# Kernel tuning notes

Hardware: AMD Instinct MI355X
Metric: run time of the kernel (lower is better)

The kernel has to match this reference:

```python
import jax, jax.numpy as jnp
import numpy as np

B, C1, C2, K, H, W = 2, 256, 256, 3, 64, 64
PAD = 1
EPS = 1e-5
K2 = K * K
OUT_OFF = 3 * K2  # deform_groups=1: 2*k2 offset channels + k2 mask channels


def setup_inputs() -> dict:
    key = jax.random.key(0)
    ks = jax.random.split(key, 8)
    x = jax.random.normal(ks[0], (B, C1, H, W), jnp.float32)
    # small scale so predicted offsets stay within a few pixels (realistic trained regime)
    w_off = jax.random.normal(ks[1], (OUT_OFF, C1, 3, 3), jnp.float32) * 0.01
    b_off = jax.random.normal(ks[2], (OUT_OFF,), jnp.float32) * 0.01
    w_dcn = jax.random.normal(ks[3], (C2, C1, K, K), jnp.float32) / np.sqrt(C1 * K2).astype(np.float32)
    gamma = 1.0 + 0.1 * jax.random.normal(ks[4], (C2,), jnp.float32)
    beta = 0.1 * jax.random.normal(ks[5], (C2,), jnp.float32)
    run_mean = 0.1 * jax.random.normal(ks[6], (C2,), jnp.float32)
    run_var = jax.random.uniform(ks[7], (C2,), jnp.float32, minval=0.5, maxval=1.5)
    return {"x": x, "w_off": w_off, "b_off": b_off, "w_dcn": w_dcn,
            "gamma": gamma, "beta": beta, "run_mean": run_mean, "run_var": run_var}


def _dcnv2_bn_silu(x, w_off, b_off, w_dcn, gamma, beta, run_mean, run_var):
    # offset/mask predictor: plain 3x3 conv, stride 1, pad 1
    om = jax.lax.conv_general_dilated(x, w_off, (1, 1), [(PAD, PAD), (PAD, PAD)])
    om = om + b_off[None, :, None, None]  # [B, 27, H, W]
    # mmcv channel layout: (dy, dx) interleaved per kernel tap, then mask
    offset = om[:, :2 * K2].reshape(B, K2, 2, H, W)
    mask = jax.nn.sigmoid(om[:, 2 * K2:3 * K2])  # [B, K2, H, W]
    dy, dx = offset[:, :, 0], offset[:, :, 1]     # [B, K2, H, W]

    ki = jnp.arange(K)
    tap_y = jnp.repeat(ki, K)  # [K2]
    tap_x = jnp.tile(ki, K)    # [K2]
    base_y = jnp.arange(H)[None, None, :, None] - PAD + tap_y[None, :, None, None]
    base_x = jnp.arange(W)[None, None, None, :] - PAD + tap_x[None, :, None, None]
    py = base_y.astype(x.dtype) + dy  # [B, K2, H, W] sampling rows
    px = base_x.astype(x.dtype) + dx  # [B, K2, H, W] sampling cols

    y0f = jnp.floor(py)
    x0f = jnp.floor(px)
    ly = (py - y0f)[:, None]  # [B, 1, K2, H, W]
    lx = (px - x0f)[:, None]
    y0 = y0f.astype(jnp.int32)
    x0 = x0f.astype(jnp.int32)

    x_flat = x.reshape(B, C1, H * W)

    def gather(yi, xi):
        valid = ((yi >= 0) & (yi < H) & (xi >= 0) & (xi < W)).astype(x.dtype)
        idx = jnp.clip(yi, 0, H - 1) * W + jnp.clip(xi, 0, W - 1)  # [B, K2, H, W]
        v = jnp.take_along_axis(x_flat, idx.reshape(B, 1, -1), axis=2)
        return v.reshape(B, C1, K2, H, W) * valid[:, None]

    v00 = gather(y0, x0)
    v01 = gather(y0, x0 + 1)
    v10 = gather(y0 + 1, x0)
    v11 = gather(y0 + 1, x0 + 1)
    vals = (v00 * (1 - ly) * (1 - lx) + v01 * (1 - ly) * lx
            + v10 * ly * (1 - lx) + v11 * ly * lx)
    vals = vals * mask[:, None]  # modulated

    out = jnp.einsum('bckhw,ock->bohw', vals, w_dcn.reshape(C2, C1, K2))

    # BatchNorm (inference, running stats) + SiLU
    inv = gamma / jnp.sqrt(run_var + EPS)
    y = out * inv[None, :, None, None] + (beta - run_mean * inv)[None, :, None, None]
    return y * jax.nn.sigmoid(y)


def reference(x, w_off, b_off, w_dcn, gamma, beta, run_mean, run_var):
    return _dcnv2_bn_silu(x, w_off, b_off, w_dcn, gamma, beta, run_mean, run_var)
```

## Files before the change

### kernel.cpp

```cpp
#include <hip/hip_runtime.h>
#include <hip/hip_bf16.h>
#include <math.h>

typedef __bf16 bf16x8 __attribute__((ext_vector_type(8)));
typedef float  f32x4  __attribute__((ext_vector_type(4)));

#define BB 2
#define C1 256
#define C2 256
#define HH 64
#define WW 64
#define HW 4096
#define OCH 27
#define EPSV 1e-5f

#define WBF_OFF  0u
#define WOFF_OFF 1179648u
#define XT_OFF   1327104u

__global__ __launch_bounds__(256) void prep_kernel(
    const float* __restrict__ x, const float* __restrict__ w_dcn,
    const float* __restrict__ w_off, __bf16* __restrict__ xT,
    __bf16* __restrict__ wbfS, __bf16* __restrict__ woffS)
{
    __shared__ __bf16 tile[64][72];
    const int bi = blockIdx.x, tid = threadIdx.x;

    if (bi < 512) {
        const int b = bi >> 8;
        const int ht = (bi & 255) >> 2;
        const int ct = bi & 3;
        const int hw_l = tid & 63, cg = tid >> 6;
        const float* src = x + ((size_t)(b * 256 + ct * 64 + cg * 16) << 12)
                             + ht * 64 + hw_l;
        #pragma unroll
        for (int i = 0; i < 16; i++)
            tile[hw_l][cg * 16 + i] = (__bf16)src[(size_t)i << 12];
        __syncthreads();
        const int hw_o = tid >> 2, cq = tid & 3;
        __bf16* dst = xT + ((size_t)(b * HW + ht * 64 + hw_o) << 8)
                         + ct * 64 + cq * 16;
        *(bf16x8*)dst       = *(const bf16x8*)&tile[hw_o][cq * 16];
        *(bf16x8*)(dst + 8) = *(const bf16x8*)&tile[hw_o][cq * 16 + 8];
    } else if (bi < 800) {
        int t = (bi - 512) * 256 + tid;
        int l = t & 63;
        int nb = (t >> 6) & 15;
        int ks = (t >> 10) & 1;
        int kb = t >> 11;
        int o = nb * 16 + (l & 15);
        int kq = (l >> 4) & 3;
        bf16x8 v;
        #pragma unroll
        for (int j = 0; j < 8; j++) {
            int K = kb * 64 + ks * 32 + kq * 8 + j;
            v[j] = (__bf16)w_dcn[o * 2304 + (K & 255) * 9 + (K >> 8)];
        }
        *(bf16x8*)(wbfS + (size_t)t * 8) = v;
    } else {
        int t = (bi - 800) * 256 + tid;
        int l = t & 63;
        int nf = (t >> 6) & 1;
        int ks = (t >> 7) & 1;
        int kb = t >> 8;
        int o = nf * 16 + (l & 15);
        int kq = (l >> 4) & 3;
        bf16x8 v;
        #pragma unroll
        for (int j = 0; j < 8; j++) {
            int K = kb * 64 + ks * 32 + kq * 8 + j;
            v[j] = (o < OCH) ? (__bf16)w_off[o * 2304 + (K & 255) * 9 + (K >> 8)]
                             : (__bf16)0.f;
        }
        *(bf16x8*)(woffS + (size_t)t * 8) = v;
    }
}

union SU {
    float sD[4][16][33];
    float sC[2][16][136];
};

__global__ __launch_bounds__(256, 4) void fused_kernel(
    const __bf16* __restrict__ xT, const __bf16* __restrict__ wbfS,
    const __bf16* __restrict__ woffS, const float* __restrict__ b_off,
    const float* __restrict__ gamma, const float* __restrict__ beta,
    const float* __restrict__ rmean, const float* __restrict__ rvar,
    float* __restrict__ out)
{
    __shared__ SU u;
    __shared__ float  sOm[32][16];
    __shared__ int4   sO[9][16];
    __shared__ float4 sW[9][16];

    const int tid = threadIdx.x, wv = tid >> 6, lane = tid & 63;
    const int bi = blockIdx.x;
    const int xcd = bi & 7, rr = bi >> 3;
    const int g = xcd * 64 + (rr >> 1);
    const int nHalf = rr & 1;
    const int pixBase = g * 16;
    const int b = pixBase >> 12;
    const int hwBase = pixBase & 4095;
    const int h = hwBase >> 6, w0 = hwBase & 63;
    const int n15 = lane & 15, q4 = lane >> 4;

    const char* xb = (const char*)xT + ((size_t)b << 12) * 512;

    {
        f32x4 acc2[2];
        #pragma unroll
        for (int j = 0; j < 2; j++) acc2[j] = (f32x4){0.f, 0.f, 0.f, 0.f};

        for (int i = 0; i < 9; i++) {
            const int kb = wv * 9 + i;
            const int k = kb >> 2, cc = kb & 3;
            const int kh = k / 3, kw = k % 3;
            const int hh = h + kh - 1;
            const int ww = w0 + n15 + kw - 1;
            const bool valid = (hh >= 0) && (hh < HH) && (ww >= 0) && (ww < WW);
            const int hc = min(max(hh, 0), HH - 1);
            const int wc = min(max(ww, 0), WW - 1);
            const char* src = xb + (size_t)(hc * WW + wc) * 512
                                 + (cc * 64 + q4 * 8) * 2;
            bf16x8 af[2];
            af[0] = *(const bf16x8*)src;
            af[1] = *(const bf16x8*)(src + 64);
            if (!valid) {
                #pragma unroll
                for (int j = 0; j < 8; j++) {
                    af[0][j] = (__bf16)0.f; af[1][j] = (__bf16)0.f;
                }
            }
            #pragma unroll
            for (int nf = 0; nf < 2; nf++) {
                #pragma unroll
                for (int ks = 0; ks < 2; ks++) {
                    bf16x8 bfr = *(const bf16x8*)(woffS
                        + ((size_t)(((kb * 2 + ks) * 2 + nf) * 64 + lane)) * 8);
                    acc2[nf] = __builtin_amdgcn_mfma_f32_16x16x32_bf16(
                        af[ks], bfr, acc2[nf], 0, 0, 0);
                }
            }
        }
        #pragma unroll
        for (int nf = 0; nf < 2; nf++)
            #pragma unroll
            for (int r = 0; r < 4; r++)
                u.sD[wv][q4 * 4 + r][nf * 16 + n15] = acc2[nf][r];
    }
    __syncthreads();
    for (int t = tid; t < OCH * 16; t += 256) {
        int oc = t >> 4, p = t & 15;
        sOm[oc][p] = b_off[oc] + u.sD[0][p][oc] + u.sD[1][p][oc]
                               + u.sD[2][p][oc] + u.sD[3][p][oc];
    }
    __syncthreads();

    if (tid < 144) {
        int k = tid >> 4, p = tid & 15;
        float dy = sOm[2 * k][p];
        float dx = sOm[2 * k + 1][p];
        float mm = sOm[18 + k][p];
        mm = 1.f / (1.f + __expf(-mm));
        float py = (float)(h - 1 + k / 3) + dy;
        float px = (float)(w0 + p - 1 + k % 3) + dx;
        float y0f = floorf(py), x0f = floorf(px);
        float ly = py - y0f, lx = px - x0f;
        int y0 = (int)y0f, x0 = (int)x0f;
        int yc0 = min(max(y0, 0), HH - 1),     yc1 = min(max(y0 + 1, 0), HH - 1);
        int xc0 = min(max(x0, 0), WW - 1),     xc1 = min(max(x0 + 1, 0), WW - 1);
        float vy0 = (y0 >= 0 && y0 < HH) ? 1.f : 0.f;
        float vy1 = (y0 + 1 >= 0 && y0 + 1 < HH) ? 1.f : 0.f;
        float vx0 = (x0 >= 0 && x0 < WW) ? 1.f : 0.f;
        float vx1 = (x0 + 1 >= 0 && x0 + 1 < WW) ? 1.f : 0.f;
        sO[k][p] = (int4){(yc0 * WW + xc0) * 512, (yc0 * WW + xc1) * 512,
                          (yc1 * WW + xc0) * 512, (yc1 * WW + xc1) * 512};
        sW[k][p] = (float4){(1.f - ly) * (1.f - lx) * vy0 * vx0 * mm,
                            (1.f - ly) * lx         * vy0 * vx1 * mm,
                            ly         * (1.f - lx) * vy1 * vx0 * mm,
                            ly         * lx         * vy1 * vx1 * mm};
    }
    __syncthreads();

    f32x4 acc[8];
    #pragma unroll
    for (int j = 0; j < 8; j++) acc[j] = (f32x4){0.f, 0.f, 0.f, 0.f};

    for (int i = 0; i < 9; i++) {
        const int kb = wv * 9 + i;
        const int k = kb >> 2, cc = kb & 3;
        const int4   O = sO[k][n15];
        const float4 W = sW[k][n15];
        const char* base = xb + (cc * 64 + q4 * 8) * 2;

        bf16x8 af[2];
        #pragma unroll
        for (int ks = 0; ks < 2; ks++) {
            const char* bc = base + ks * 64;
            bf16x8 c00 = *(const bf16x8*)(bc + O.x);
            bf16x8 c01 = *(const bf16x8*)(bc + O.y);
            bf16x8 c10 = *(const bf16x8*)(bc + O.z);
            bf16x8 c11 = *(const bf16x8*)(bc + O.w);
            bf16x8 a;
            #pragma unroll
            for (int j = 0; j < 8; j++) {
                float v = W.x * (float)c00[j] + W.y * (float)c01[j]
                        + W.z * (float)c10[j] + W.w * (float)c11[j];
                a[j] = (__bf16)v;
            }
            af[ks] = a;
        }

        #pragma unroll
        for (int half = 0; half < 2; half++) {
            bf16x8 bfr[4][2];
            #pragma unroll
            for (int nb = 0; nb < 4; nb++)
                #pragma unroll
                for (int ks = 0; ks < 2; ks++)
                    bfr[nb][ks] = *(const bf16x8*)(wbfS
                        + ((size_t)(((kb * 2 + ks) * 16 + nHalf * 8 + half * 4 + nb)
                                    * 64 + lane)) * 8);
            #pragma unroll
            for (int nb = 0; nb < 4; nb++)
                #pragma unroll
                for (int ks = 0; ks < 2; ks++)
                    acc[half * 4 + nb] = __builtin_amdgcn_mfma_f32_16x16x32_bf16(
                        af[ks], bfr[nb][ks], acc[half * 4 + nb], 0, 0, 0);
        }
    }

    if (wv < 2) {
        #pragma unroll
        for (int nb = 0; nb < 8; nb++)
            #pragma unroll
            for (int r = 0; r < 4; r++)
                u.sC[wv][q4 * 4 + r][nb * 16 + n15] = acc[nb][r];
    }
    __syncthreads();
    if (wv >= 2) {
        #pragma unroll
        for (int nb = 0; nb < 8; nb++)
            #pragma unroll
            for (int r = 0; r < 4; r++)
                u.sC[wv - 2][q4 * 4 + r][nb * 16 + n15] += acc[nb][r];
    }
    __syncthreads();

    const int px = tid & 15, og = tid >> 4;
    float* ob = out + ((size_t)b * C2 << 12) + hwBase + px;
    #pragma unroll
    for (int ii = 0; ii < 8; ii++) {
        int col = og * 8 + ii;
        int o = nHalf * 128 + col;
        float s = u.sC[0][px][col] + u.sC[1][px][col];
        float inv = gamma[o] * rsqrtf(rvar[o] + EPSV);
        float sh = beta[o] - rmean[o] * inv;
        float y = s * inv + sh;
        ob[(size_t)o << 12] = y * (1.f / (1.f + __expf(-y)));
    }
}

extern "C" void kernel_launch(void* const* d_in, const int* in_sizes, int n_in,
                              void* d_out, int out_size, void* d_ws, size_t ws_size,
                              hipStream_t stream) {
    const float* x      = (const float*)d_in[0];
    const float* w_off  = (const float*)d_in[1];
    const float* b_off  = (const float*)d_in[2];
    const float* w_dcn  = (const float*)d_in[3];
    const float* gamma  = (const float*)d_in[4];
    const float* beta   = (const float*)d_in[5];
    const float* rmean  = (const float*)d_in[6];
    const float* rvar   = (const float*)d_in[7];
    float* out = (float*)d_out;

    char* ws = (char*)d_ws;
    __bf16* wbfS  = (__bf16*)(ws + WBF_OFF);
    __bf16* woffS = (__bf16*)(ws + WOFF_OFF);
    __bf16* xT    = (__bf16*)(ws + XT_OFF);

    prep_kernel<<<836, 256, 0, stream>>>(x, w_dcn, w_off, xT, wbfS, woffS);
    fused_kernel<<<1024, 256, 0, stream>>>(xT, wbfS, woffS, b_off,
                                           gamma, beta, rmean, rvar, out);
}
```

Before: 141.5 us.

## Compute all output channels per block and stage w_dcn repack through LDS

The fused kernel now has each block compute all 256 output channels for its 16 pixels instead of half. This removes the duplicated offset conv, bilinear sampling and gather work that the two channel-half blocks used to repeat, at the cost of twice the accumulator registers and lower occupancy (the occupancy hint in launch bounds is dropped). Separately, the weight repack in the prep kernel now reads w_dcn with coalesced float4 loads into shared memory and scatters from there, replacing strided scalar global reads.

```diff
diff --git a/kernel.cpp b/kernel.cpp
--- a/kernel.cpp
+++ b/kernel.cpp
@@ -24,6 +24,7 @@
     __bf16* __restrict__ wbfS, __bf16* __restrict__ woffS)
 {
     __shared__ __bf16 tile[64][72];
+    __shared__ __bf16 lw[16][584];
     const int bi = blockIdx.x, tid = threadIdx.x;
 
     if (bi < 512) {
@@ -42,23 +43,37 @@
                          + ct * 64 + cq * 16;
         *(bf16x8*)dst       = *(const bf16x8*)&tile[hw_o][cq * 16];
         *(bf16x8*)(dst + 8) = *(const bf16x8*)&tile[hw_o][cq * 16 + 8];
-    } else if (bi < 800) {
-        int t = (bi - 512) * 256 + tid;
-        int l = t & 63;
-        int nb = (t >> 6) & 15;
-        int ks = (t >> 10) & 1;
-        int kb = t >> 11;
-        int o = nb * 16 + (l & 15);
-        int kq = (l >> 4) & 3;
-        bf16x8 v;
-        #pragma unroll
-        for (int j = 0; j < 8; j++) {
-            int K = kb * 64 + ks * 32 + kq * 8 + j;
-            v[j] = (__bf16)w_dcn[o * 2304 + (K & 255) * 9 + (K >> 8)];
-        }
-        *(bf16x8*)(wbfS + (size_t)t * 8) = v;
+    } else if (bi < 576) {
+        const int b2 = bi - 512;
+        const int nb = b2 >> 2, qtr = b2 & 3;
+        #pragma unroll
+        for (int ii = 0; ii < 9; ii++) {
+            int m = tid + 256 * ii;
+            int base = m * 4;
+            int o_l = base / 576;
+            int f = base - o_l * 576;
+            float4 v = *(const float4*)(w_dcn
+                + (size_t)(nb * 16 + o_l) * 2304 + qtr * 576 + f);
+            lw[o_l][f]     = (__bf16)v.x;
+            lw[o_l][f + 1] = (__bf16)v.y;
+            lw[o_l][f + 2] = (__bf16)v.z;
+            lw[o_l][f + 3] = (__bf16)v.w;
+        }
+        __syncthreads();
+        #pragma unroll
+        for (int ii = 0; ii < 36; ii++) {
+            int e = ii * 256 + tid;
+            int seg = e >> 9, s = e & 511;
+            int lane = s >> 3, j = s & 7;
+            int tap = seg >> 1, ks = seg & 1;
+            int kb = tap * 4 + qtr;
+            int o_l = lane & 15, kq = (lane >> 4) & 3;
+            int c_local = ks * 32 + kq * 8 + j;
+            wbfS[((size_t)(((kb * 2 + ks) * 16 + nb) * 64 + lane)) * 8 + j]
+                = lw[o_l][c_local * 9 + tap];
+        }
     } else {
-        int t = (bi - 800) * 256 + tid;
+        int t = (bi - 576) * 256 + tid;
         int l = t & 63;
         int nf = (t >> 6) & 1;
         int ks = (t >> 7) & 1;
@@ -78,10 +93,10 @@
 
 union SU {
     float sD[4][16][33];
-    float sC[2][16][136];
+    float sC[2][16][260];
 };
 
-__global__ __launch_bounds__(256, 4) void fused_kernel(
+__global__ __launch_bounds__(256) void fused_kernel(
     const __bf16* __restrict__ xT, const __bf16* __restrict__ wbfS,
     const __bf16* __restrict__ woffS, const float* __restrict__ b_off,
     const float* __restrict__ gamma, const float* __restrict__ beta,
@@ -94,10 +109,7 @@
     __shared__ float4 sW[9][16];
 
     const int tid = threadIdx.x, wv = tid >> 6, lane = tid & 63;
-    const int bi = blockIdx.x;
-    const int xcd = bi & 7, rr = bi >> 3;
-    const int g = xcd * 64 + (rr >> 1);
-    const int nHalf = rr & 1;
+    const int g = (blockIdx.x & 7) * 64 + (blockIdx.x >> 3);
     const int pixBase = g * 16;
     const int b = pixBase >> 12;
     const int hwBase = pixBase & 4095;
@@ -182,9 +194,9 @@
     }
     __syncthreads();
 
-    f32x4 acc[8];
+    f32x4 acc[16];
     #pragma unroll
-    for (int j = 0; j < 8; j++) acc[j] = (f32x4){0.f, 0.f, 0.f, 0.f};
+    for (int j = 0; j < 16; j++) acc[j] = (f32x4){0.f, 0.f, 0.f, 0.f};
 
     for (int i = 0; i < 9; i++) {
         const int kb = wv * 9 + i;
@@ -213,26 +225,25 @@
 
         #pragma unroll
         for (int half = 0; half < 2; half++) {
-            bf16x8 bfr[4][2];
-            #pragma unroll
-            for (int nb = 0; nb < 4; nb++)
+            bf16x8 bfr[8][2];
+            #pragma unroll
+            for (int nb = 0; nb < 8; nb++)
                 #pragma unroll
                 for (int ks = 0; ks < 2; ks++)
                     bfr[nb][ks] = *(const bf16x8*)(wbfS
-                        + ((size_t)(((kb * 2 + ks) * 16 + nHalf * 8 + half * 4 + nb)
-                                    * 64 + lane)) * 8);
-            #pragma unroll
-            for (int nb = 0; nb < 4; nb++)
+                        + ((size_t)(((kb * 2 + ks) * 16 + half * 8 + nb) * 64 + lane)) * 8);
+            #pragma unroll
+            for (int nb = 0; nb < 8; nb++)
                 #pragma unroll
                 for (int ks = 0; ks < 2; ks++)
-                    acc[half * 4 + nb] = __builtin_amdgcn_mfma_f32_16x16x32_bf16(
-                        af[ks], bfr[nb][ks], acc[half * 4 + nb], 0, 0, 0);
+                    acc[half * 8 + nb] = __builtin_amdgcn_mfma_f32_16x16x32_bf16(
+                        af[ks], bfr[nb][ks], acc[half * 8 + nb], 0, 0, 0);
         }
     }
 
     if (wv < 2) {
         #pragma unroll
-        for (int nb = 0; nb < 8; nb++)
+        for (int nb = 0; nb < 16; nb++)
             #pragma unroll
             for (int r = 0; r < 4; r++)
                 u.sC[wv][q4 * 4 + r][nb * 16 + n15] = acc[nb][r];
@@ -240,7 +251,7 @@
     __syncthreads();
     if (wv >= 2) {
         #pragma unroll
-        for (int nb = 0; nb < 8; nb++)
+        for (int nb = 0; nb < 16; nb++)
             #pragma unroll
             for (int r = 0; r < 4; r++)
                 u.sC[wv - 2][q4 * 4 + r][nb * 16 + n15] += acc[nb][r];
@@ -250,10 +261,9 @@
     const int px = tid & 15, og = tid >> 4;
     float* ob = out + ((size_t)b * C2 << 12) + hwBase + px;
     #pragma unroll
-    for (int ii = 0; ii < 8; ii++) {
-        int col = og * 8 + ii;
-        int o = nHalf * 128 + col;
-        float s = u.sC[0][px][col] + u.sC[1][px][col];
+    for (int ii = 0; ii < 16; ii++) {
+        int o = og * 16 + ii;
+        float s = u.sC[0][px][o] + u.sC[1][px][o];
         float inv = gamma[o] * rsqrtf(rvar[o] + EPSV);
         float sh = beta[o] - rmean[o] * inv;
         float y = s * inv + sh;
@@ -279,7 +289,7 @@
     __bf16* woffS = (__bf16*)(ws + WOFF_OFF);
     __bf16* xT    = (__bf16*)(ws + XT_OFF);
 
-    prep_kernel<<<836, 256, 0, stream>>>(x, w_dcn, w_off, xT, wbfS, woffS);
-    fused_kernel<<<1024, 256, 0, stream>>>(xT, wbfS, woffS, b_off,
-                                           gamma, beta, rmean, rvar, out);
+    prep_kernel<<<612, 256, 0, stream>>>(x, w_dcn, w_off, xT, wbfS, woffS);
+    fused_kernel<<<512, 256, 0, stream>>>(xT, wbfS, woffS, b_off,
+                                          gamma, beta, rmean, rvar, out);
 }
```

After: 122.3 us. -13.6%, faster.
